# Performance work log

Measured on AMD Instinct MI355X. Metric: run time of the kernel, lower is better.

The kernel has to match this reference:

```python
import jax, jax.numpy as jnp
import numpy as np

DIM = 1024
HEADS = 16
DIM_HEAD = 64
INNER = HEADS * DIM_HEAD  # 1024
EPS = 1e-5


def setup_inputs() -> dict:
    key = jax.random.key(0)
    ks = jax.random.split(key, 8)
    B, N = 4, 2048
    s = 0.02
    return {
        "query": jax.random.normal(ks[0], (B, N, DIM), jnp.float32),
        "key_": jax.random.normal(ks[1], (B, N, DIM), jnp.float32),
        "value": jax.random.normal(ks[2], (B, N, DIM), jnp.float32),
        "Wq": jax.random.normal(ks[3], (DIM, INNER), jnp.float32) * s,
        "Wk": jax.random.normal(ks[4], (DIM, INNER), jnp.float32) * s,
        "Wv": jax.random.normal(ks[5], (DIM, INNER), jnp.float32) * s,
        "Wo": jax.random.normal(ks[6], (INNER, DIM), jnp.float32) * s,
        "bo": jnp.zeros((DIM,), jnp.float32),
        "gamma": jnp.ones((DIM,), jnp.float32),
        "beta": jnp.zeros((DIM,), jnp.float32),
    }


def reference(query, key_, value, Wq, Wk, Wv, Wo, bo, gamma, beta):
    B, N, _ = query.shape
    scale = DIM_HEAD ** (-0.5)
    # project and split heads: [B, H, N, Dh]
    q = (query @ Wq).reshape(B, N, HEADS, DIM_HEAD).transpose(0, 2, 1, 3)
    k = (key_ @ Wk).reshape(B, N, HEADS, DIM_HEAD).transpose(0, 2, 1, 3)
    v = (value @ Wv).reshape(B, N, HEADS, DIM_HEAD).transpose(0, 2, 1, 3)
    dots = jnp.einsum("bhnd,bhmd->bhnm", q, k) * scale  # [B,H,N,N]
    attn = jax.nn.softmax(dots, axis=-1)
    out = jnp.einsum("bhnm,bhmd->bhnd", attn, v)
    out = out.transpose(0, 2, 1, 3).reshape(B, N, INNER)
    out = out @ Wo + bo  # dropout p=0.0 is identity
    # LayerNorm over last dim
    mu = out.mean(-1, keepdims=True)
    var = ((out - mu) ** 2).mean(-1, keepdims=True)
    normed = (out - mu) * jax.lax.rsqrt(var + EPS) * gamma + beta
    return normed + query
```

## Files before the change

kernel.cpp:

```cpp
#include <hip/hip_runtime.h>
#include <stdint.h>

#define K_DIM 1024
#define B_SZ 4
#define N_SEQ 2048
#define HEADS 16
#define DH 64
#define M_TOT (B_SZ * N_SEQ)

typedef __bf16 bf16x8 __attribute__((ext_vector_type(8)));
typedef __bf16 bf16x4 __attribute__((ext_vector_type(4)));
typedef __bf16 bf16x2 __attribute__((ext_vector_type(2)));
typedef float f32x4 __attribute__((ext_vector_type(4)));
typedef float f32x16 __attribute__((ext_vector_type(16)));

typedef const uint32_t __attribute__((address_space(1))) gas_u32;
typedef uint32_t __attribute__((address_space(3))) las_u32;

#define CE_SCALE 0.1803368801f

__device__ __forceinline__ uint16_t f2bf(float f) {
  uint32_t u = __float_as_uint(f);
  u += 0x7FFFu + ((u >> 16) & 1u);
  return (uint16_t)(u >> 16);
}

__device__ __forceinline__ void gld_lds16(const uint16_t* g, uint16_t* lds) {
  __builtin_amdgcn_global_load_lds((gas_u32*)g, (las_u32*)lds, 16, 0, 0);
}

__device__ __forceinline__ uint32_t pkbf(float a, float b) {
  bf16x2 t;
  t[0] = (__bf16)a;
  t[1] = (__bf16)b;
  return __builtin_bit_cast(uint32_t, t);
}

__device__ __forceinline__ void pswap(uint32_t& a, uint32_t& b) {
  asm("v_permlane32_swap_b32 %0, %1" : "+v"(a), "+v"(b));
}

__global__ __launch_bounds__(256) void prep_k(const float* __restrict__ aq,
                                              const float* __restrict__ ak,
                                              const float* __restrict__ av,
                                              const float* __restrict__ w0,
                                              const float* __restrict__ w1,
                                              const float* __restrict__ w2,
                                              const float* __restrict__ w3,
                                              uint16_t* __restrict__ xdst,
                                              uint16_t* __restrict__ wdst) {
  __shared__ float tile[32][33];
  const int bid = blockIdx.x;
  const int tid = threadIdx.x;
  if (bid < 3 * 8192) {
    const int z = bid >> 13;
    const int xb = bid & 8191;
    const float* src = (z == 0) ? aq : (z == 1) ? ak : av;
    uint16_t* dst = xdst + (size_t)z * M_TOT * K_DIM;
    const int i = xb * 256 + tid;
    float4 v = ((const float4*)src)[i];
    ushort4 o;
    o.x = f2bf(v.x); o.y = f2bf(v.y); o.z = f2bf(v.z); o.w = f2bf(v.w);
    ((ushort4*)dst)[i] = o;
  } else {
    const int t = bid - 3 * 8192;
    const int z = t >> 10;
    const int rb = t & 1023;
    const float* src = (z == 0) ? w0 : (z == 1) ? w1 : (z == 2) ? w2 : w3;
    uint16_t* dst = wdst + (size_t)z * 1024 * 1024;
    const int tx = tid & 31, ty = tid >> 5;
    const int bx = (rb & 31) * 32, by = (rb >> 5) * 32;
#pragma unroll
    for (int i = 0; i < 32; i += 8)
      tile[ty + i][tx] = src[(size_t)(by + ty + i) * 1024 + bx + tx];
    __syncthreads();
#pragma unroll
    for (int i = 0; i < 32; i += 8)
      dst[(size_t)(bx + ty + i) * 1024 + by + tx] = f2bf(tile[tx][ty + i]);
  }
}

template <int MODE>
__global__ __launch_bounds__(256, 2) void gemm_bf16(const uint16_t* __restrict__ A,
                                                    const uint16_t* __restrict__ BT,
                                                    void* __restrict__ Cout,
                                                    const float* __restrict__ bias) {
  __shared__ __align__(16) uint16_t As[2][128 * 32];
  __shared__ __align__(16) uint16_t Bs[2][128 * 32];
  const int tid = threadIdx.x;
  const int wave = tid >> 6, lane = tid & 63;
  const int g = lane >> 4, c16 = lane & 15;

  const int bid = blockIdx.x;
  const int xcd = bid & 7;
  const int l = bid >> 3;
  const int z = (MODE == 3) ? (l >> 6) : 0;
  const int r = l & 63;
  const int n0 = (r & 7) * 128;
  const int m0 = (xcd * 8 + (r >> 3)) * 128;

  const int wr = wave >> 1, wc = wave & 1;
  float scale = 1.f;
  if (MODE == 3) {
    A += (size_t)z * M_TOT * K_DIM;
    BT += (size_t)z * 1024 * 1024;
    scale = (z == 0) ? CE_SCALE : 1.f;
  }

  const f32x4 fzero = {0.f, 0.f, 0.f, 0.f};
  f32x4 acc[4][4];
#pragma unroll
  for (int i = 0; i < 4; ++i)
#pragma unroll
    for (int j = 0; j < 4; ++j) acc[i][j] = fzero;

  const int srow = wave * 32 + (lane >> 2);
  const int scol = (((lane & 3) ^ ((srow >> 1) & 3)) * 8);
  const uint16_t* ag0 = A + (size_t)(m0 + srow) * K_DIM + scol;
  const uint16_t* ag1 = A + (size_t)(m0 + srow + 16) * K_DIM + scol;
  const uint16_t* bg0 = BT + (size_t)(n0 + srow) * K_DIM + scol;
  const uint16_t* bg1 = BT + (size_t)(n0 + srow + 16) * K_DIM + scol;
  const int lofa0 = (wave * 32) * 32;
  const int lofa1 = (wave * 32 + 16) * 32;

  const int rk = (c16 >> 1) & 3;

  gld_lds16(ag0, &As[0][lofa0]);
  gld_lds16(ag1, &As[0][lofa1]);
  gld_lds16(bg0, &Bs[0][lofa0]);
  gld_lds16(bg1, &Bs[0][lofa1]);
  __syncthreads();

  int cur = 0;
  for (int kt = 0; kt < K_DIM / 32; ++kt) {
    if (kt + 1 < K_DIM / 32) {
      const int nxt = cur ^ 1;
      gld_lds16(ag0 + (kt + 1) * 32, &As[nxt][lofa0]);
      gld_lds16(ag1 + (kt + 1) * 32, &As[nxt][lofa1]);
      gld_lds16(bg0 + (kt + 1) * 32, &Bs[nxt][lofa0]);
      gld_lds16(bg1 + (kt + 1) * 32, &Bs[nxt][lofa1]);
    }
    bf16x8 avec[4], bvec[4];
#pragma unroll
    for (int i = 0; i < 4; ++i)
      avec[i] = *(const bf16x8*)&As[cur][(wr * 64 + i * 16 + c16) * 32 + ((g ^ rk) << 3)];
#pragma unroll
    for (int j = 0; j < 4; ++j)
      bvec[j] = *(const bf16x8*)&Bs[cur][(wc * 64 + j * 16 + c16) * 32 + ((g ^ rk) << 3)];
#pragma unroll
    for (int i = 0; i < 4; ++i)
#pragma unroll
      for (int j = 0; j < 4; ++j)
        acc[i][j] = __builtin_amdgcn_mfma_f32_16x16x32_bf16(avec[i], bvec[j], acc[i][j], 0, 0, 0);
    __syncthreads();
    cur ^= 1;
  }

#pragma unroll
  for (int i = 0; i < 4; ++i) {
#pragma unroll
    for (int j = 0; j < 4; ++j) {
      const int col = n0 + wc * 64 + j * 16 + c16;
      if (MODE == 3 && z == 2) {
        const int h = col >> 6, d = col & 63;
        const int row0 = m0 + wr * 64 + i * 16 + g * 4;
        const int b = row0 >> 11, n = row0 & 2047;
        ushort4 o;
        o.x = f2bf(acc[i][j][0]); o.y = f2bf(acc[i][j][1]);
        o.z = f2bf(acc[i][j][2]); o.w = f2bf(acc[i][j][3]);
        *(ushort4*)&((uint16_t*)Cout)[(size_t)2 * M_TOT * 1024 +
                                      (((size_t)(b * HEADS + h)) * DH + d) * N_SEQ + n] = o;
      } else {
#pragma unroll
        for (int r2 = 0; r2 < 4; ++r2) {
          const int row = m0 + wr * 64 + i * 16 + g * 4 + r2;
          if (MODE == 3) {
            const int b = row >> 11, n = row & 2047;
            const int h = col >> 6, d = col & 63;
            ((uint16_t*)Cout)[(size_t)z * M_TOT * 1024 +
                              (((size_t)(b * HEADS + h)) * N_SEQ + n) * DH + d] =
                f2bf(acc[i][j][r2] * scale);
          } else {
            ((float*)Cout)[(size_t)row * 1024 + col] = acc[i][j][r2] + bias[col];
          }
        }
      }
    }
  }
}

__global__ __launch_bounds__(256, 2) void attention_k(const uint16_t* __restrict__ qm,
                                                      const uint16_t* __restrict__ km,
                                                      const uint16_t* __restrict__ vtm,
                                                      uint16_t* __restrict__ om) {
  __shared__ __align__(16) uint16_t Ks[2 * 64 * 64];
  __shared__ __align__(16) uint16_t Vs[2 * 64 * 64];
  const int tid = threadIdx.x;
  const int wave = tid >> 6, lane = tid & 63;
  const int lrow = lane & 31;
  const int hi = lane >> 5;

  const int bid = blockIdx.x;
  const int xcd = bid & 7;
  const int l0 = bid >> 3;
  const int bh = xcd * 8 + (l0 & 7);
  const int qblk = l0 >> 3;
  const int b = bh >> 4, h = bh & 15;
  const int q0w = qblk * 256 + wave * 64;

  const uint16_t* qbase = qm + (size_t)bh * N_SEQ * DH;
  const uint16_t* kbase = km + (size_t)bh * N_SEQ * DH;
  const uint16_t* vbase = vtm + (size_t)bh * DH * N_SEQ;

  bf16x8 qf[2][4];
#pragma unroll
  for (int qs = 0; qs < 2; ++qs) {
    const uint16_t* qp = qbase + (size_t)(q0w + qs * 32 + lrow) * DH + hi * 8;
#pragma unroll
    for (int step = 0; step < 4; ++step) qf[qs][step] = *(const bf16x8*)(qp + step * 16);
  }

  int koff[2][4];
  int voff[2][2][2];
#pragma unroll
  for (int ks = 0; ks < 2; ++ks) {
    const int krow = ks * 32 + lrow;
#pragma unroll
    for (int step = 0; step < 4; ++step)
      koff[ks][step] = krow * 64 + ((((step << 1) | hi) ^ (krow & 7)) << 3);
#pragma unroll
    for (int s = 0; s < 2; ++s)
#pragma unroll
      for (int dt = 0; dt < 2; ++dt)
        voff[ks][s][dt] =
            (dt * 32 + lrow) * 64 + ((((ks << 2) | (s << 1) | hi) ^ (lrow & 7)) << 3);
  }

  f32x16 oacc[2][2];
#pragma unroll
  for (int qs = 0; qs < 2; ++qs)
#pragma unroll
    for (int dt = 0; dt < 2; ++dt)
#pragma unroll
      for (int i = 0; i < 16; ++i) oacc[qs][dt][i] = 0.f;
  float l[2] = {0.f, 0.f};

  const int ch = tid & 7;
  const int krow0 = tid >> 3, krow1 = 32 + (tid >> 3);
  const int kdst0 = krow0 * 64 + ((ch ^ (krow0 & 7)) << 3);
  const int kdst1 = krow1 * 64 + ((ch ^ (krow1 & 7)) << 3);

  uint4 kp0, kp1, vp0, vp1;
  kp0 = *(const uint4*)&kbase[(size_t)tid * 8];
  kp1 = *(const uint4*)&kbase[(size_t)(256 + tid) * 8];
  vp0 = *(const uint4*)&vbase[(size_t)krow0 * N_SEQ + ch * 8];
  vp1 = *(const uint4*)&vbase[(size_t)krow1 * N_SEQ + ch * 8];
  *(uint4*)&Ks[kdst0] = kp0;
  *(uint4*)&Ks[kdst1] = kp1;
  *(uint4*)&Vs[kdst0] = vp0;
  *(uint4*)&Vs[kdst1] = vp1;
  __syncthreads();

  for (int t = 0; t < N_SEQ / 64; ++t) {
    const int cur = t & 1;
    if (t < N_SEQ / 64 - 1) {
      const size_t ko = (size_t)(t + 1) * 4096;
      const int vc = (t + 1) * 64;
      kp0 = *(const uint4*)&kbase[ko + (size_t)tid * 8];
      kp1 = *(const uint4*)&kbase[ko + (size_t)(256 + tid) * 8];
      vp0 = *(const uint4*)&vbase[(size_t)krow0 * N_SEQ + vc + ch * 8];
      vp1 = *(const uint4*)&vbase[(size_t)krow1 * N_SEQ + vc + ch * 8];
    }
    const uint16_t* ksp = &Ks[cur * 4096];
    const uint16_t* vsp = &Vs[cur * 4096];

#pragma unroll
    for (int ks = 0; ks < 2; ++ks) {
      bf16x8 kf[4];
#pragma unroll
      for (int step = 0; step < 4; ++step) kf[step] = *(const bf16x8*)&ksp[koff[ks][step]];

      f32x16 z[2];
#pragma unroll
      for (int qs = 0; qs < 2; ++qs)
#pragma unroll
        for (int i = 0; i < 16; ++i) z[qs][i] = 0.f;

      __builtin_amdgcn_s_setprio(1);
#pragma unroll
      for (int step = 0; step < 4; ++step)
        z[0] = __builtin_amdgcn_mfma_f32_32x32x16_bf16(kf[step], qf[0][step], z[0], 0, 0, 0);
#pragma unroll
      for (int step = 0; step < 4; ++step)
        z[1] = __builtin_amdgcn_mfma_f32_32x32x16_bf16(kf[step], qf[1][step], z[1], 0, 0, 0);
      __builtin_amdgcn_s_setprio(0);

      uint32_t pa[2][2][4];
#pragma unroll
      for (int qs = 0; qs < 2; ++qs) {
        float p[16];
#pragma unroll
        for (int r = 0; r < 16; ++r) p[r] = __builtin_amdgcn_exp2f(z[qs][r]);
        l[qs] += (((p[0] + p[1]) + (p[2] + p[3])) + ((p[4] + p[5]) + (p[6] + p[7]))) +
                 (((p[8] + p[9]) + (p[10] + p[11])) + ((p[12] + p[13]) + (p[14] + p[15])));
#pragma unroll
        for (int s = 0; s < 2; ++s) {
          uint32_t w0 = pkbf(p[s * 8 + 0], p[s * 8 + 1]);
          uint32_t w1 = pkbf(p[s * 8 + 2], p[s * 8 + 3]);
          uint32_t w2 = pkbf(p[s * 8 + 4], p[s * 8 + 5]);
          uint32_t w3 = pkbf(p[s * 8 + 6], p[s * 8 + 7]);
          pswap(w0, w2);
          pswap(w1, w3);
          pa[qs][s][0] = w0; pa[qs][s][1] = w1; pa[qs][s][2] = w2; pa[qs][s][3] = w3;
        }
      }

      bf16x8 vf[2][2];
#pragma unroll
      for (int s = 0; s < 2; ++s)
#pragma unroll
        for (int dt = 0; dt < 2; ++dt) vf[s][dt] = *(const bf16x8*)&vsp[voff[ks][s][dt]];

      __builtin_amdgcn_s_setprio(1);
#pragma unroll
      for (int s = 0; s < 2; ++s)
#pragma unroll
        for (int qs = 0; qs < 2; ++qs) {
          uint4 u;
          u.x = pa[qs][s][0]; u.y = pa[qs][s][1]; u.z = pa[qs][s][2]; u.w = pa[qs][s][3];
          const bf16x8 paf = __builtin_bit_cast(bf16x8, u);
          oacc[qs][0] = __builtin_amdgcn_mfma_f32_32x32x16_bf16(paf, vf[s][0], oacc[qs][0], 0, 0, 0);
          oacc[qs][1] = __builtin_amdgcn_mfma_f32_32x32x16_bf16(paf, vf[s][1], oacc[qs][1], 0, 0, 0);
        }
      __builtin_amdgcn_s_setprio(0);
    }

    if (t < N_SEQ / 64 - 1) {
      *(uint4*)&Ks[(cur ^ 1) * 4096 + kdst0] = kp0;
      *(uint4*)&Ks[(cur ^ 1) * 4096 + kdst1] = kp1;
      *(uint4*)&Vs[(cur ^ 1) * 4096 + kdst0] = vp0;
      *(uint4*)&Vs[(cur ^ 1) * 4096 + kdst1] = vp1;
      __syncthreads();
    }
  }

#pragma unroll
  for (int qs = 0; qs < 2; ++qs) l[qs] += __shfl_xor(l[qs], 32);

#pragma unroll
  for (int qs = 0; qs < 2; ++qs) {
#pragma unroll
    for (int r = 0; r < 16; ++r) {
      const int ql = (r & 3) + 8 * (r >> 2) + 4 * hi;
      const float lr = __shfl(l[qs], ql);
      const float inv = 1.f / lr;
      const int row = q0w + qs * 32 + ql;
      const size_t base = ((size_t)b * N_SEQ + row) * 1024 + h * 64;
      om[base + lrow] = f2bf(oacc[qs][0][r] * inv);
      om[base + 32 + lrow] = f2bf(oacc[qs][1][r] * inv);
    }
  }
}

__global__ __launch_bounds__(256) void ln_res_k(const float* __restrict__ proj,
                                                const float* __restrict__ query,
                                                const float* __restrict__ gamma,
                                                const float* __restrict__ beta,
                                                float* __restrict__ out) {
  const int row = blockIdx.x;
  const int tid = threadIdx.x;
  const size_t base = (size_t)row * 1024 + tid * 4;
  float4 v = *(const float4*)(proj + base);
  float s = v.x + v.y + v.z + v.w;
  float s2 = v.x * v.x + v.y * v.y + v.z * v.z + v.w * v.w;
#pragma unroll
  for (int off = 1; off < 64; off <<= 1) {
    s += __shfl_xor(s, off);
    s2 += __shfl_xor(s2, off);
  }
  __shared__ float red[8];
  const int wave = tid >> 6, lane = tid & 63;
  if (lane == 0) { red[wave] = s; red[4 + wave] = s2; }
  __syncthreads();
  s = red[0] + red[1] + red[2] + red[3];
  s2 = red[4] + red[5] + red[6] + red[7];
  const float mu = s * (1.f / 1024.f);
  const float var = fmaxf(s2 * (1.f / 1024.f) - mu * mu, 0.f);
  const float rstd = rsqrtf(var + 1e-5f);
  float4 gq = *(const float4*)(gamma + tid * 4);
  float4 bq = *(const float4*)(beta + tid * 4);
  float4 qq = *(const float4*)(query + base);
  float4 o;
  o.x = (v.x - mu) * rstd * gq.x + bq.x + qq.x;
  o.y = (v.y - mu) * rstd * gq.y + bq.y + qq.y;
  o.z = (v.z - mu) * rstd * gq.z + bq.z + qq.z;
  o.w = (v.w - mu) * rstd * gq.w + bq.w + qq.w;
  *(float4*)(out + base) = o;
}

extern "C" void kernel_launch(void* const* d_in, const int* in_sizes, int n_in,
                              void* d_out, int out_size, void* d_ws, size_t ws_size,
                              hipStream_t stream) {
  (void)in_sizes; (void)n_in; (void)out_size; (void)ws_size;
  const float* query = (const float*)d_in[0];
  const float* key_ = (const float*)d_in[1];
  const float* value = (const float*)d_in[2];
  const float* Wq = (const float*)d_in[3];
  const float* Wk = (const float*)d_in[4];
  const float* Wv = (const float*)d_in[5];
  const float* Wo = (const float*)d_in[6];
  const float* bo = (const float*)d_in[7];
  const float* gamma = (const float*)d_in[8];
  const float* beta = (const float*)d_in[9];
  float* out = (float*)d_out;

  const size_t NELEM = (size_t)M_TOT * 1024;
  uint16_t* wsp = (uint16_t*)d_ws;
  uint16_t* WqT = wsp;
  uint16_t* WoT = WqT + 3 * 1024 * 1024;
  uint16_t* xq = WqT + 4 * 1024 * 1024;
  uint16_t* qb = xq + 3 * NELEM;
  uint16_t* attnO = xq;
  float* proj = (float*)(xq + NELEM);

  prep_k<<<28672, 256, 0, stream>>>(query, key_, value, Wq, Wk, Wv, Wo, xq, WqT);

  gemm_bf16<3><<<1536, 256, 0, stream>>>(xq, WqT, qb, nullptr);

  attention_k<<<512, 256, 0, stream>>>(qb, qb + NELEM, qb + 2 * NELEM, attnO);

  gemm_bf16<1><<<512, 256, 0, stream>>>(attnO, WoT, proj, bo);

  ln_res_k<<<8192, 256, 0, stream>>>(proj, query, gamma, beta, out);
}
```

Before: 337.5 us.

## Enlarge GEMM tiles to 256x128 with BK=64 and 512-thread blocks

The bf16 GEMM moves from 128x128 tiles with a K-step of 32 and 256 threads to 256x128 tiles with a K-step of 64 and 8 waves per block. Block-index swizzling and the XOR LDS layout are reworked to match. The aim is to halve the number of barrier iterations and raise operand reuse per block, cutting global traffic and sync overhead. The cost is 96KB of LDS per block, which limits occupancy, and fewer blocks in flight, which can hurt wave-level latency hiding.

```diff
diff --git a/kernel.cpp b/kernel.cpp
--- a/kernel.cpp
+++ b/kernel.cpp
@@ -81,23 +81,23 @@
 }
 
 template <int MODE>
-__global__ __launch_bounds__(256, 2) void gemm_bf16(const uint16_t* __restrict__ A,
+__global__ __launch_bounds__(512, 2) void gemm_bf16(const uint16_t* __restrict__ A,
                                                     const uint16_t* __restrict__ BT,
                                                     void* __restrict__ Cout,
                                                     const float* __restrict__ bias) {
-  __shared__ __align__(16) uint16_t As[2][128 * 32];
-  __shared__ __align__(16) uint16_t Bs[2][128 * 32];
+  __shared__ __align__(16) uint16_t As[2][256 * 64];
+  __shared__ __align__(16) uint16_t Bs[2][128 * 64];
   const int tid = threadIdx.x;
   const int wave = tid >> 6, lane = tid & 63;
   const int g = lane >> 4, c16 = lane & 15;
 
   const int bid = blockIdx.x;
-  const int xcd = bid & 7;
-  const int l = bid >> 3;
-  const int z = (MODE == 3) ? (l >> 6) : 0;
-  const int r = l & 63;
-  const int n0 = (r & 7) * 128;
-  const int m0 = (xcd * 8 + (r >> 3)) * 128;
+  const int z = (MODE == 3) ? (bid >> 8) : 0;
+  const int r = bid & 255;
+  const int xcd = r & 7;
+  const int l = r >> 3;
+  const int m0 = (xcd * 4 + (l >> 3)) * 256;
+  const int n0 = (l & 7) * 128;
 
   const int wr = wave >> 1, wc = wave & 1;
   float scale = 1.f;
@@ -114,44 +114,58 @@
 #pragma unroll
     for (int j = 0; j < 4; ++j) acc[i][j] = fzero;
 
-  const int srow = wave * 32 + (lane >> 2);
-  const int scol = (((lane & 3) ^ ((srow >> 1) & 3)) * 8);
-  const uint16_t* ag0 = A + (size_t)(m0 + srow) * K_DIM + scol;
-  const uint16_t* ag1 = A + (size_t)(m0 + srow + 16) * K_DIM + scol;
-  const uint16_t* bg0 = BT + (size_t)(n0 + srow) * K_DIM + scol;
-  const uint16_t* bg1 = BT + (size_t)(n0 + srow + 16) * K_DIM + scol;
-  const int lofa0 = (wave * 32) * 32;
-  const int lofa1 = (wave * 32 + 16) * 32;
-
-  const int rk = (c16 >> 1) & 3;
-
-  gld_lds16(ag0, &As[0][lofa0]);
-  gld_lds16(ag1, &As[0][lofa1]);
-  gld_lds16(bg0, &Bs[0][lofa0]);
-  gld_lds16(bg1, &Bs[0][lofa1]);
+  const int lsub = lane >> 3;
+  const int ch = lane & 7;
+  const uint16_t* agp[4];
+  int aldo[4];
+#pragma unroll
+  for (int q = 0; q < 4; ++q) {
+    const int rowA = (wave * 4 + q) * 8 + lsub;
+    agp[q] = A + (size_t)(m0 + rowA) * K_DIM + ((ch ^ (rowA & 7)) * 8);
+    aldo[q] = (wave * 4 + q) * 512;
+  }
+  const uint16_t* bgp[2];
+  int bldo[2];
+#pragma unroll
+  for (int q = 0; q < 2; ++q) {
+    const int rowB = (wave * 2 + q) * 8 + lsub;
+    bgp[q] = BT + (size_t)(n0 + rowB) * K_DIM + ((ch ^ (rowB & 7)) * 8);
+    bldo[q] = (wave * 2 + q) * 512;
+  }
+
+  const int rk = c16 & 7;
+
+#pragma unroll
+  for (int q = 0; q < 4; ++q) gld_lds16(agp[q], &As[0][aldo[q]]);
+#pragma unroll
+  for (int q = 0; q < 2; ++q) gld_lds16(bgp[q], &Bs[0][bldo[q]]);
   __syncthreads();
 
   int cur = 0;
-  for (int kt = 0; kt < K_DIM / 32; ++kt) {
-    if (kt + 1 < K_DIM / 32) {
+  for (int kt = 0; kt < K_DIM / 64; ++kt) {
+    if (kt + 1 < K_DIM / 64) {
       const int nxt = cur ^ 1;
-      gld_lds16(ag0 + (kt + 1) * 32, &As[nxt][lofa0]);
-      gld_lds16(ag1 + (kt + 1) * 32, &As[nxt][lofa1]);
-      gld_lds16(bg0 + (kt + 1) * 32, &Bs[nxt][lofa0]);
-      gld_lds16(bg1 + (kt + 1) * 32, &Bs[nxt][lofa1]);
-    }
-    bf16x8 avec[4], bvec[4];
-#pragma unroll
-    for (int i = 0; i < 4; ++i)
-      avec[i] = *(const bf16x8*)&As[cur][(wr * 64 + i * 16 + c16) * 32 + ((g ^ rk) << 3)];
-#pragma unroll
-    for (int j = 0; j < 4; ++j)
-      bvec[j] = *(const bf16x8*)&Bs[cur][(wc * 64 + j * 16 + c16) * 32 + ((g ^ rk) << 3)];
-#pragma unroll
-    for (int i = 0; i < 4; ++i)
+#pragma unroll
+      for (int q = 0; q < 4; ++q) gld_lds16(agp[q] + (kt + 1) * 64, &As[nxt][aldo[q]]);
+#pragma unroll
+      for (int q = 0; q < 2; ++q) gld_lds16(bgp[q] + (kt + 1) * 64, &Bs[nxt][bldo[q]]);
+    }
+#pragma unroll
+    for (int ksub = 0; ksub < 2; ++ksub) {
+      const int co = (((ksub << 2) | g) ^ rk) << 3;
+      bf16x8 avec[4], bvec[4];
+#pragma unroll
+      for (int i = 0; i < 4; ++i)
+        avec[i] = *(const bf16x8*)&As[cur][(wr * 64 + i * 16 + c16) * 64 + co];
 #pragma unroll
       for (int j = 0; j < 4; ++j)
-        acc[i][j] = __builtin_amdgcn_mfma_f32_16x16x32_bf16(avec[i], bvec[j], acc[i][j], 0, 0, 0);
+        bvec[j] = *(const bf16x8*)&Bs[cur][(wc * 64 + j * 16 + c16) * 64 + co];
+#pragma unroll
+      for (int i = 0; i < 4; ++i)
+#pragma unroll
+        for (int j = 0; j < 4; ++j)
+          acc[i][j] = __builtin_amdgcn_mfma_f32_16x16x32_bf16(avec[i], bvec[j], acc[i][j], 0, 0, 0);
+    }
     __syncthreads();
     cur ^= 1;
   }
@@ -425,11 +439,11 @@
 
   prep_k<<<28672, 256, 0, stream>>>(query, key_, value, Wq, Wk, Wv, Wo, xq, WqT);
 
-  gemm_bf16<3><<<1536, 256, 0, stream>>>(xq, WqT, qb, nullptr);
+  gemm_bf16<3><<<768, 512, 0, stream>>>(xq, WqT, qb, nullptr);
 
   attention_k<<<512, 256, 0, stream>>>(qb, qb + NELEM, qb + 2 * NELEM, attnO);
 
-  gemm_bf16<1><<<512, 256, 0, stream>>>(attnO, WoT, proj, bo);
+  gemm_bf16<1><<<256, 512, 0, stream>>>(attnO, WoT, proj, bo);
 
   ln_res_k<<<8192, 256, 0, stream>>>(proj, query, gamma, beta, out);
 }
```

Result: no change. 337.4 us (-0.0%).

## Deepen GEMM LDS pipeline to four buffers with prefetch distance two

Applied to the files above, without the earlier changes.

Replaces the double-buffered GEMM main loop with a four-slot LDS ring and keeps two tiles in flight, using explicit vmcnt waits and one barrier per iteration instead of a trailing syncthreads. The aim is to hide global-to-LDS load latency better and cut barrier stalls. LDS use doubles to 64 KB per block, which may limit the two-blocks-per-CU occupancy. Only the bare s_barrier orders reuse of a slot, so correctness depends on the four-slot distance being enough.

```diff
diff --git a/kernel.cpp b/kernel.cpp
--- a/kernel.cpp
+++ b/kernel.cpp
@@ -85,8 +85,8 @@
                                                     const uint16_t* __restrict__ BT,
                                                     void* __restrict__ Cout,
                                                     const float* __restrict__ bias) {
-  __shared__ __align__(16) uint16_t As[2][128 * 32];
-  __shared__ __align__(16) uint16_t Bs[2][128 * 32];
+  __shared__ __align__(16) uint16_t As[4][128 * 32];
+  __shared__ __align__(16) uint16_t Bs[4][128 * 32];
   const int tid = threadIdx.x;
   const int wave = tid >> 6, lane = tid & 63;
   const int g = lane >> 4, c16 = lane & 15;
@@ -125,36 +125,50 @@
 
   const int rk = (c16 >> 1) & 3;
 
-  gld_lds16(ag0, &As[0][lofa0]);
-  gld_lds16(ag1, &As[0][lofa1]);
-  gld_lds16(bg0, &Bs[0][lofa0]);
-  gld_lds16(bg1, &Bs[0][lofa1]);
-  __syncthreads();
-
-  int cur = 0;
-  for (int kt = 0; kt < K_DIM / 32; ++kt) {
-    if (kt + 1 < K_DIM / 32) {
-      const int nxt = cur ^ 1;
-      gld_lds16(ag0 + (kt + 1) * 32, &As[nxt][lofa0]);
-      gld_lds16(ag1 + (kt + 1) * 32, &As[nxt][lofa1]);
-      gld_lds16(bg0 + (kt + 1) * 32, &Bs[nxt][lofa0]);
-      gld_lds16(bg1 + (kt + 1) * 32, &Bs[nxt][lofa1]);
-    }
-    bf16x8 avec[4], bvec[4];
-#pragma unroll
-    for (int i = 0; i < 4; ++i)
-      avec[i] = *(const bf16x8*)&As[cur][(wr * 64 + i * 16 + c16) * 32 + ((g ^ rk) << 3)];
-#pragma unroll
-    for (int j = 0; j < 4; ++j)
-      bvec[j] = *(const bf16x8*)&Bs[cur][(wc * 64 + j * 16 + c16) * 32 + ((g ^ rk) << 3)];
-#pragma unroll
-    for (int i = 0; i < 4; ++i)
-#pragma unroll
-      for (int j = 0; j < 4; ++j)
-        acc[i][j] = __builtin_amdgcn_mfma_f32_16x16x32_bf16(avec[i], bvec[j], acc[i][j], 0, 0, 0);
-    __syncthreads();
-    cur ^= 1;
-  }
+#define STAGE_TILE(T)                                      \
+  do {                                                     \
+    const int sb_ = (T) & 3;                               \
+    gld_lds16(ag0 + (T) * 32, &As[sb_][lofa0]);            \
+    gld_lds16(ag1 + (T) * 32, &As[sb_][lofa1]);            \
+    gld_lds16(bg0 + (T) * 32, &Bs[sb_][lofa0]);            \
+    gld_lds16(bg1 + (T) * 32, &Bs[sb_][lofa1]);            \
+  } while (0)
+
+#define COMPUTE_TILE(T)                                                                   \
+  do {                                                                                    \
+    const int cb_ = (T) & 3;                                                              \
+    bf16x8 avec[4], bvec[4];                                                              \
+    _Pragma("unroll") for (int i = 0; i < 4; ++i) avec[i] =                               \
+        *(const bf16x8*)&As[cb_][(wr * 64 + i * 16 + c16) * 32 + ((g ^ rk) << 3)];        \
+    _Pragma("unroll") for (int j = 0; j < 4; ++j) bvec[j] =                               \
+        *(const bf16x8*)&Bs[cb_][(wc * 64 + j * 16 + c16) * 32 + ((g ^ rk) << 3)];        \
+    _Pragma("unroll") for (int i = 0; i < 4; ++i) _Pragma("unroll") for (int j = 0; j < 4;\
+                                                                         ++j) acc[i][j] = \
+        __builtin_amdgcn_mfma_f32_16x16x32_bf16(avec[i], bvec[j], acc[i][j], 0, 0, 0);    \
+  } while (0)
+
+  STAGE_TILE(0);
+  STAGE_TILE(1);
+
+  const int NT = K_DIM / 32;
+  for (int t = 0; t < NT - 2; ++t) {
+    STAGE_TILE(t + 2);
+    asm volatile("s_waitcnt vmcnt(8)" ::: "memory");
+    __builtin_amdgcn_sched_barrier(0);
+    __builtin_amdgcn_s_barrier();
+    COMPUTE_TILE(t);
+  }
+  asm volatile("s_waitcnt vmcnt(4)" ::: "memory");
+  __builtin_amdgcn_sched_barrier(0);
+  __builtin_amdgcn_s_barrier();
+  COMPUTE_TILE(NT - 2);
+  asm volatile("s_waitcnt vmcnt(0)" ::: "memory");
+  __builtin_amdgcn_sched_barrier(0);
+  __builtin_amdgcn_s_barrier();
+  COMPUTE_TILE(NT - 1);
+
+#undef STAGE_TILE
+#undef COMPUTE_TILE
 
 #pragma unroll
   for (int i = 0; i < 4; ++i) {
```

Result: no change. 339.9 us (+0.7%).
